# Optimization experiments

Measured on AMD Instinct MI355X. Metric: run time of the kernel, lower is better.

Reference implementation:

```python
import jax, jax.numpy as jnp
import numpy as np

H = 128  # per-direction hidden size; bidirectional output = 256


def sru_layer(x, W, b):
    """One bidirectional SRU layer (use_selu=1).
    x: (L, B, n_in); W: (n_in, 2H*k); b: (4H,) = [f-bias(2H), r-bias(2H)].
    """
    L, B, n_in = x.shape
    k = W.shape[1] // (2 * H)  # 4 if n_in != 2H else 3
    U = (x @ W).reshape(L, B, 2, H, k)  # (L,B,dir,H,k)
    bf = b[: 2 * H].reshape(2, H)
    br = b[2 * H :].reshape(2, H)
    # highway input: learned projection (k==4) or the input itself split per direction
    xp = U[..., 3] if k == 4 else x.reshape(L, B, 2, H)
    # time-reverse the backward direction so a single scan serves both
    Us = jnp.stack([U[:, :, 0, :, :3], U[::-1, :, 1, :, :3]], axis=2)  # (L,B,2,H,3)
    xps = jnp.stack([xp[:, :, 0], xp[::-1, :, 1]], axis=2)  # (L,B,2,H)

    def step(c, t):
        u, xpt = t
        xt = u[..., 0]
        f = jax.nn.sigmoid(u[..., 1] + bf)
        r = jax.nn.sigmoid(u[..., 2] + br)
        c = f * c + (1.0 - f) * xt
        h = r * jax.nn.selu(c) + (1.0 - r) * xpt
        return c, h

    c0 = jnp.zeros((B, 2, H), x.dtype)
    _, hs = jax.lax.scan(step, c0, (Us, xps))  # hs: (L,B,2,H)
    # un-reverse backward direction, concat directions -> (L,B,2H)
    return jnp.concatenate([hs[:, :, 0], hs[::-1, :, 1]], axis=-1)


def setup_inputs() -> dict:
    key = jax.random.key(0)
    ks = jax.random.split(key, 6)
    L, B, D = 1024, 64, 128
    inp = {
        "input": jax.random.normal(ks[0], (L, B, D), jnp.float32),
        "W0": jax.random.normal(ks[1], (D, 4 * 2 * H), jnp.float32) / np.sqrt(D),
        "b0": jnp.zeros((4 * H,), jnp.float32),
        "gamma": jnp.ones((2 * H,), jnp.float32),
        "beta": jnp.zeros((2 * H,), jnp.float32),
    }
    for i, kk in zip((1, 2, 3), ks[2:5]):
        inp[f"W{i}"] = jax.random.normal(kk, (2 * H, 3 * 2 * H), jnp.float32) / np.sqrt(2 * H)
        inp[f"b{i}"] = jnp.zeros((4 * H,), jnp.float32)
    return inp


def reference(input, W0, b0, W1, b1, W2, b2, W3, b3, gamma, beta):
    x = sru_layer(input, W0, b0)
    x = sru_layer(x, W1, b1)
    x = sru_layer(x, W2, b2)
    x = sru_layer(x, W3, b3)  # (L,B,256)
    # permute(1,2,0) + avg_pool1d over full length + squeeze == mean over time
    feats = jnp.mean(x, axis=0)  # (B,256)
    mu = jnp.mean(feats, axis=-1, keepdims=True)
    var = jnp.mean(jnp.square(feats - mu), axis=-1, keepdims=True)
    return (feats - mu) / jnp.sqrt(var + 1e-5) * gamma + beta
```

## Files before the change

kernel.cpp:

```cpp
#include <hip/hip_runtime.h>
#include <math.h>

#define HID 128
#define LSEQ 1024
#define NB 64
#define SUB 32
#define NQG (LSEQ / SUB)
#define NCH 16384

typedef __attribute__((ext_vector_type(4))) float f32x4;
typedef __attribute__((ext_vector_type(8))) short bf16x8;
typedef __attribute__((ext_vector_type(8))) unsigned short u16x8;
typedef __attribute__((ext_vector_type(4))) unsigned short u16x4;

__device__ __forceinline__ unsigned short f2bf(float x) {
    union { float f; unsigned int u; } a; a.f = x;
    unsigned int r = a.u + 0x7FFFu + ((a.u >> 16) & 1u);
    return (unsigned short)(r >> 16);
}
__device__ __forceinline__ float bf2f(unsigned short h) {
    union { float f; unsigned int u; } a; a.u = ((unsigned int)h) << 16;
    return a.f;
}
__device__ __forceinline__ float sigmoidf_(float x) { return 1.0f / (1.0f + __expf(-x)); }
__device__ __forceinline__ float seluf_(float x) {
    const float sc = 1.0507009873554805f, al = 1.6732632423543772f;
    return x > 0.0f ? sc * x : sc * al * (__expf(x) - 1.0f);
}

__device__ __forceinline__ void gload16(const unsigned short* g, unsigned short* l) {
    __builtin_amdgcn_global_load_lds(
        (const __attribute__((address_space(1))) unsigned int*)g,
        (__attribute__((address_space(3))) unsigned int*)l, 16, 0, 0);
}

__global__ __launch_bounds__(256) void conv_wt(const float* __restrict__ W,
                                               unsigned short* __restrict__ Wt,
                                               int K, int N, int kw) {
    int idx = blockIdx.x * 256 + threadIdx.x;
    if (idx >= K * N) return;
    int k = idx / N, n = idx - k * N;
    const int dir = n / (128 * kw);
    const int rem = n - dir * 128 * kw;
    const int h = rem / kw, j = rem - h * kw;
    const int np = dir * 128 * kw + j * 128 + h;
    Wt[(size_t)np * K + k] = f2bf(W[idx]);
}

__global__ __launch_bounds__(256) void conv_in(const float* __restrict__ in,
                                               unsigned short* __restrict__ outp,
                                               int n4) {
    int idx = blockIdx.x * 256 + threadIdx.x;
    if (idx >= n4) return;
    const float4 v = *reinterpret_cast<const float4*>(in + (size_t)idx * 4);
    u16x4 w;
    w[0] = f2bf(v.x); w[1] = f2bf(v.y); w[2] = f2bf(v.z); w[3] = f2bf(v.w);
    *(u16x4*)(outp + (size_t)idx * 4) = w;
}

template <int K, int NC>
__global__ __launch_bounds__(256, 2) void gemm_v9(const unsigned short* __restrict__ A,
                                                  const unsigned short* __restrict__ Bt,
                                                  unsigned short* __restrict__ C) {
    constexpr int NN = NC / 128;
    constexpr int NT = K / 64;
    constexpr int NSTEP = 4 * NT;
    __shared__ __align__(16) unsigned short smB[NT * 8192];

    const int bid = blockIdx.x;
    const int mi = bid & 7;
    const int tt = bid >> 3;
    const int n = tt % NN;
    const int mg = (tt / NN) * 8 + mi;
    const int mb = mg * 512;
    const int n0 = n * 128;

    const int tid = threadIdx.x;
    const int w = tid >> 6, l = tid & 63;
    const int rlo = l & 15, g = l >> 4;
    const int kswz = (rlo & 7) * 8;

#pragma unroll
    for (int kt = 0; kt < NT; ++kt)
#pragma unroll
        for (int cc = 0; cc < 4; ++cc) {
            const int col = cc * 32 + (tid >> 3);
            const int kxb = (tid & 7) ^ ((tid >> 3) & 7);
            gload16(Bt + (size_t)(n0 + col) * K + kt * 64 + kxb * 8,
                    &smB[kt * 8192 + cc * 2048 + tid * 8]);
        }

    const unsigned short* gA = A + ((size_t)mb + w * 32 + rlo) * K + g * 8;

    bf16x8 af[2][2][2];
    auto loadA = [&](int s, int buf) {
        const int mt = s / NT, kt = s % NT;
        const unsigned short* p = gA + (size_t)mt * 128 * K + kt * 64;
#pragma unroll
        for (int mf = 0; mf < 2; ++mf)
#pragma unroll
            for (int kk = 0; kk < 2; ++kk)
                af[buf][mf][kk] = *(const bf16x8*)(p + (size_t)mf * 16 * K + kk * 32);
    };

    loadA(0, 0);
    __syncthreads();

    f32x4 acc[2][8];
#pragma unroll
    for (int s = 0; s < NSTEP; ++s) {
        const int mt = s / NT, kt = s % NT, cur = s & 1;
        if (kt == 0) {
#pragma unroll
            for (int mf = 0; mf < 2; ++mf)
#pragma unroll
                for (int nf = 0; nf < 8; ++nf) acc[mf][nf] = (f32x4){0.f, 0.f, 0.f, 0.f};
        }
        if (s + 1 < NSTEP) loadA(s + 1, cur ^ 1);
#pragma unroll
        for (int kk = 0; kk < 2; ++kk) {
            const int koff = (kk * 32 + g * 8) ^ kswz;
            bf16x8 bff[8];
#pragma unroll
            for (int nf = 0; nf < 8; ++nf)
                bff[nf] = *(const bf16x8*)(&smB[kt * 8192 + (nf * 16 + rlo) * 64 + koff]);
#pragma unroll
            for (int mf = 0; mf < 2; ++mf)
#pragma unroll
                for (int nf = 0; nf < 8; ++nf)
                    acc[mf][nf] = __builtin_amdgcn_mfma_f32_16x16x32_bf16(
                        bff[nf], af[cur][mf][kk], acc[mf][nf], 0, 0, 0);
        }
        if (kt == NT - 1) {
            const int rowb = mb + mt * 128 + w * 32;
#pragma unroll
            for (int mf = 0; mf < 2; ++mf) {
                const size_t rbase = (size_t)(rowb + mf * 16 + rlo) * NC + n0 + g * 4;
#pragma unroll
                for (int nf = 0; nf < 8; ++nf) {
                    u16x4 v;
                    v[0] = f2bf(acc[mf][nf][0]); v[1] = f2bf(acc[mf][nf][1]);
                    v[2] = f2bf(acc[mf][nf][2]); v[3] = f2bf(acc[mf][nf][3]);
                    *(u16x4*)(&C[rbase + nf * 16]) = v;
                }
            }
        }
    }
}

template <int NC>
__global__ __launch_bounds__(256) void scanA(const unsigned short* __restrict__ U,
                                             const float* __restrict__ bias,
                                             float* __restrict__ aArr,
                                             float* __restrict__ bArr,
                                             int dirbase, int dbstride,
                                             int chmask, int chshift, int T) {
    const int gid = blockIdx.x * 256 + threadIdx.x;
    const int fc = gid & chmask;
    const int q = gid >> chshift;
    const int dir = dirbase + (fc >> 13);
    const int b = (fc >> 7) & 63, h = fc & 127;
    const int dbase = (fc >> 13) * dbstride;
    const float bfb = bias[dir * HID + h];

    float aa = 1.0f, cc = 0.0f;
#pragma unroll 4
    for (int i = 0; i < SUB; ++i) {
        const int s = q * SUB + i;
        const int t = dir ? (T - 1 - s) : s;
        const size_t m = (size_t)t * NB + b;
        const float u0 = bf2f(U[m * NC + dbase + h]);
        const float u1 = bf2f(U[m * NC + dbase + 128 + h]);
        const float f = sigmoidf_(u1 + bfb);
        cc = f * cc + (1.0f - f) * u0;
        aa *= f;
    }
    const int fcg = dir * 8192 + (fc & 8191);
    aArr[(size_t)q * NCH + fcg] = aa;
    bArr[(size_t)q * NCH + fcg] = cc;
}

template <int Q>
__global__ __launch_bounds__(256) void scanB(const float* __restrict__ aArr,
                                             const float* __restrict__ bArr,
                                             float* __restrict__ cin,
                                             float* __restrict__ carry,
                                             int init, int fcg0) {
    const int fcg = fcg0 + blockIdx.x * 256 + threadIdx.x;
    float a[Q], bb[Q];
#pragma unroll
    for (int q = 0; q < Q; ++q) {
        a[q]  = aArr[(size_t)q * NCH + fcg];
        bb[q] = bArr[(size_t)q * NCH + fcg];
    }
    float c = init ? 0.0f : carry[fcg];
#pragma unroll
    for (int q = 0; q < Q; ++q) {
        cin[(size_t)q * NCH + fcg] = c;
        c = a[q] * c + bb[q];
    }
    carry[fcg] = c;
}

template <int NC, bool XP_FROM_U, bool ACC>
__global__ __launch_bounds__(256) void scanC(const unsigned short* __restrict__ U,
                                             const unsigned short* __restrict__ Xprev,
                                             const float* __restrict__ bias,
                                             const float* __restrict__ cin,
                                             unsigned short* __restrict__ Xout,
                                             float* __restrict__ part,
                                             int dirbase, int dbstride,
                                             int chmask, int chshift,
                                             int T, int t0, int qg0) {
    const int gid = blockIdx.x * 256 + threadIdx.x;
    const int fc = gid & chmask;
    const int q = gid >> chshift;
    const int dir = dirbase + (fc >> 13);
    const int b = (fc >> 7) & 63, h = fc & 127;
    const int dbase = (fc >> 13) * dbstride;
    const float bfb = bias[dir * HID + h];
    const float brb = bias[2 * HID + dir * HID + h];
    const int fcg = dir * 8192 + (fc & 8191);

    float c = cin[(size_t)q * NCH + fcg];
    float psum = 0.0f;
#pragma unroll 4
    for (int i = 0; i < SUB; ++i) {
        const int s = q * SUB + i;
        const int t = dir ? (T - 1 - s) : s;
        const size_t m = (size_t)t * NB + b;
        const size_t xrow = ((size_t)(t0 + t) * NB + b) * (2 * HID) + dir * HID + h;
        const float u0 = bf2f(U[m * NC + dbase + h]);
        const float u1 = bf2f(U[m * NC + dbase + 128 + h]);
        const float u2 = bf2f(U[m * NC + dbase + 256 + h]);
        float xp;
        if constexpr (XP_FROM_U) xp = bf2f(U[m * NC + dbase + 384 + h]);
        else                     xp = bf2f(Xprev[xrow]);
        const float f = sigmoidf_(u1 + bfb);
        const float r = sigmoidf_(u2 + brb);
        c = f * c + (1.0f - f) * u0;
        const float ho = r * seluf_(c) + (1.0f - r) * xp;
        if constexpr (ACC) psum += ho;
        else               Xout[xrow] = f2bf(ho);
    }
    if constexpr (ACC)
        part[(size_t)(qg0 + q) * (NB * 256) + b * 256 + dir * HID + h] = psum;
}

__global__ __launch_bounds__(256) void pool2(const float* __restrict__ part,
                                             const float* __restrict__ gamma,
                                             const float* __restrict__ beta,
                                             float* __restrict__ out) {
    const int b = blockIdx.x, chn = threadIdx.x;
    float s = 0.0f;
#pragma unroll
    for (int i = 0; i < NQG; ++i) s += part[(size_t)i * (NB * 256) + b * 256 + chn];
    const float feat = s * (1.0f / LSEQ);
    __shared__ float red[256];
    red[chn] = feat; __syncthreads();
    for (int off = 128; off > 0; off >>= 1) { if (chn < off) red[chn] += red[chn + off]; __syncthreads(); }
    const float mu = red[0] * (1.0f / 256.0f);
    __syncthreads();
    const float d = feat - mu;
    red[chn] = d * d; __syncthreads();
    for (int off = 128; off > 0; off >>= 1) { if (chn < off) red[chn] += red[chn + off]; __syncthreads(); }
    const float var = red[0] * (1.0f / 256.0f);
    out[b * 256 + chn] = d * rsqrtf(var + 1e-5f) * gamma[chn] + beta[chn];
}

extern "C" void kernel_launch(void* const* d_in, const int* in_sizes, int n_in,
                              void* d_out, int out_size, void* d_ws, size_t ws_size,
                              hipStream_t stream) {
    const float* input = (const float*)d_in[0];
    const float* gamma = (const float*)d_in[3];
    const float* beta  = (const float*)d_in[4];
    const float* Wl[4] = { (const float*)d_in[1], (const float*)d_in[5],
                           (const float*)d_in[7], (const float*)d_in[9] };
    const float* bl[4] = { (const float*)d_in[2], (const float*)d_in[6],
                           (const float*)d_in[8], (const float*)d_in[10] };
    float* out = (float*)d_out;

    char* base = (char*)d_ws;
    size_t off = 0;
    auto alloc = [&](size_t bytes) { size_t o = off; off = (off + bytes + 255) & ~(size_t)255; return o; };

    unsigned short* Wt[4];
    Wt[0] = (unsigned short*)(base + alloc((size_t)1024 * 128 * 2));
    for (int i = 1; i < 4; ++i) Wt[i] = (unsigned short*)(base + alloc((size_t)768 * 256 * 2));
    unsigned short* Xa = (unsigned short*)(base + alloc((size_t)LSEQ * NB * 256 * 2));
    unsigned short* Xb = (unsigned short*)(base + alloc((size_t)LSEQ * NB * 256 * 2));
    unsigned short* Xc = (unsigned short*)(base + alloc((size_t)LSEQ * NB * 128 * 2));
    float* carry = (float*)(base + alloc((size_t)NCH * 4));
    float* aArr  = (float*)(base + alloc((size_t)32 * NCH * 4));
    float* bArr  = (float*)(base + alloc((size_t)32 * NCH * 4));
    float* cinArr= (float*)(base + alloc((size_t)32 * NCH * 4));
    float* part  = (float*)(base + alloc((size_t)NQG * NB * 256 * 4));
    if (ws_size < off + (1u << 21)) return;
    const size_t uavail = ws_size - off;
    unsigned short* U = (unsigned short*)(base + off);

    conv_in<<<(LSEQ * NB * 128 / 4 + 255) / 256, 256, 0, stream>>>(input, Xc, LSEQ * NB * 128 / 4);
    conv_wt<<<(128 * 1024 + 255) / 256, 256, 0, stream>>>(Wl[0], Wt[0], 128, 1024, 4);
    for (int i = 1; i < 4; ++i)
        conv_wt<<<(256 * 768 + 255) / 256, 256, 0, stream>>>(Wl[i], Wt[i], 256, 768, 3);

    const unsigned short* Xin[4] = { Xc, Xa, Xb, Xa };
    unsigned short* Xout[4] = { Xa, Xb, Xa, nullptr };

    if (uavail >= (size_t)LSEQ * NB * 1024 * 2) {
        const int T = LSEQ, Q = T / SUB;
        const dim3 sgrid(NCH * Q / 256);
        for (int layer = 0; layer < 4; ++layer) {
            const int kw = (layer == 0) ? 4 : 3;
            const int dbstride = 128 * kw;
            if (layer == 0)
                gemm_v9<128, 1024><<<dim3(8 * 128), 256, 0, stream>>>(Xin[0], Wt[0], U);
            else
                gemm_v9<256, 768><<<dim3(6 * 128), 256, 0, stream>>>(Xin[layer], Wt[layer], U);
            if (layer == 0)
                scanA<1024><<<sgrid, 256, 0, stream>>>(U, bl[0], aArr, bArr, 0, dbstride,
                                                       NCH - 1, 14, T);
            else
                scanA<768><<<sgrid, 256, 0, stream>>>(U, bl[layer], aArr, bArr, 0, dbstride,
                                                      NCH - 1, 14, T);
            scanB<32><<<NCH / 256, 256, 0, stream>>>(aArr, bArr, cinArr, carry, 1, 0);
            if (layer == 0)
                scanC<1024, true, false><<<sgrid, 256, 0, stream>>>(
                    U, nullptr, bl[0], cinArr, Xout[0], nullptr, 0, dbstride, NCH - 1, 14, T, 0, 0);
            else if (layer < 3)
                scanC<768, false, false><<<sgrid, 256, 0, stream>>>(
                    U, Xin[layer], bl[layer], cinArr, Xout[layer], nullptr, 0, dbstride,
                    NCH - 1, 14, T, 0, 0);
            else
                scanC<768, false, true><<<sgrid, 256, 0, stream>>>(
                    U, Xin[3], bl[3], cinArr, nullptr, part, 0, dbstride, NCH - 1, 14, T, 0, 0);
        }
    } else {
        int T = 0;
        for (int t = 512; t >= 64; t >>= 1)
            if ((size_t)t * NB * 512 * 2 <= uavail) { T = t; break; }
        if (T == 0) return;
        const int C = LSEQ / T, Q = T / SUB;
        const int nmg = T * NB / 512;
        const dim3 sgrid(8192 * Q / 256);
        for (int layer = 0; layer < 4; ++layer) {
            const int kw = (layer == 0) ? 4 : 3;
            const int K = (layer == 0) ? 128 : 256;
            const int Nc = 128 * kw;
            for (int dir = 0; dir < 2; ++dir) {
                const unsigned short* Bts = Wt[layer] + (size_t)dir * Nc * K;
                for (int cc = 0; cc < C; ++cc) {
                    const int ci = dir ? (C - 1 - cc) : cc;
                    const unsigned short* Ap = Xin[layer] + (size_t)ci * T * NB * K;
                    if (layer == 0)
                        gemm_v9<128, 512><<<dim3(4 * nmg), 256, 0, stream>>>(Ap, Bts, U);
                    else
                        gemm_v9<256, 384><<<dim3(3 * nmg), 256, 0, stream>>>(Ap, Bts, U);
                    if (layer == 0)
                        scanA<512><<<sgrid, 256, 0, stream>>>(U, bl[0], aArr, bArr, dir, 0,
                                                              8191, 13, T);
                    else
                        scanA<384><<<sgrid, 256, 0, stream>>>(U, bl[layer], aArr, bArr, dir, 0,
                                                              8191, 13, T);
                    if (Q == 16)
                        scanB<16><<<32, 256, 0, stream>>>(aArr, bArr, cinArr, carry,
                                                          cc == 0 ? 1 : 0, dir * 8192);
                    else
                        scanB<32><<<32, 256, 0, stream>>>(aArr, bArr, cinArr, carry,
                                                          cc == 0 ? 1 : 0, dir * 8192);
                    if (layer == 0)
                        scanC<512, true, false><<<sgrid, 256, 0, stream>>>(
                            U, nullptr, bl[0], cinArr, Xout[0], nullptr, dir, 0,
                            8191, 13, T, ci * T, ci * Q);
                    else if (layer < 3)
                        scanC<384, false, false><<<sgrid, 256, 0, stream>>>(
                            U, Xin[layer], bl[layer], cinArr, Xout[layer], nullptr, dir, 0,
                            8191, 13, T, ci * T, ci * Q);
                    else
                        scanC<384, false, true><<<sgrid, 256, 0, stream>>>(
                            U, Xin[3], bl[3], cinArr, nullptr, part, dir, 0,
                            8191, 13, T, ci * T, ci * Q);
                }
            }
        }
    }
    pool2<<<NB, 256, 0, stream>>>(part, gamma, beta, out);
}
```

Baseline: 415.7 us.

## Store GEMM output in MFMA-fragment tiled layout and index it from scans

The GEMM epilogue now writes each wave's accumulator fragments as contiguous 16-byte chunks in a tiled, fragment-native layout instead of scattered 8-byte row-major stores. scanA/scanC compute the matching tiled address for each (t,b,h), so consecutive threads read adjacent bf16 elements within a tile. The chunked fallback path for small workspaces is removed, and the kernel now returns early if the full U buffer does not fit. The aim is wider, better-coalesced stores in the GEMM. The cost is more complex scan indexing and possibly less contiguous reads in the scans.

Measured after the change: 634.5 us. 52.6% more time.

```diff
diff --git a/kernel.cpp b/kernel.cpp
--- a/kernel.cpp
+++ b/kernel.cpp
@@ -58,10 +58,11 @@
     *(u16x4*)(outp + (size_t)idx * 4) = w;
 }
 
+
 template <int K, int NC>
-__global__ __launch_bounds__(256, 2) void gemm_v9(const unsigned short* __restrict__ A,
-                                                  const unsigned short* __restrict__ Bt,
-                                                  unsigned short* __restrict__ C) {
+__global__ __launch_bounds__(256, 2) void gemm_v10(const unsigned short* __restrict__ A,
+                                                   const unsigned short* __restrict__ Bt,
+                                                   unsigned short* __restrict__ C) {
     constexpr int NN = NC / 128;
     constexpr int NT = K / 64;
     constexpr int NSTEP = 4 * NT;
@@ -132,61 +133,66 @@
                         bff[nf], af[cur][mf][kk], acc[mf][nf], 0, 0, 0);
         }
         if (kt == NT - 1) {
-            const int rowb = mb + mt * 128 + w * 32;
-#pragma unroll
-            for (int mf = 0; mf < 2; ++mf) {
-                const size_t rbase = (size_t)(rowb + mf * 16 + rlo) * NC + n0 + g * 4;
-#pragma unroll
-                for (int nf = 0; nf < 8; ++nf) {
-                    u16x4 v;
-                    v[0] = f2bf(acc[mf][nf][0]); v[1] = f2bf(acc[mf][nf][1]);
-                    v[2] = f2bf(acc[mf][nf][2]); v[3] = f2bf(acc[mf][nf][3]);
-                    *(u16x4*)(&C[rbase + nf * 16]) = v;
-                }
+            unsigned short* dst =
+                C + (((size_t)(mg * NN + n) * 4 + mt) * 16384) + w * 4096 + l * 8;
+#pragma unroll
+            for (int c2 = 0; c2 < 8; ++c2) {
+                const int mf = c2 >> 2, nf2 = (c2 & 3) * 2;
+                u16x8 v;
+                v[0] = f2bf(acc[mf][nf2][0]);     v[1] = f2bf(acc[mf][nf2][1]);
+                v[2] = f2bf(acc[mf][nf2][2]);     v[3] = f2bf(acc[mf][nf2][3]);
+                v[4] = f2bf(acc[mf][nf2 + 1][0]); v[5] = f2bf(acc[mf][nf2 + 1][1]);
+                v[6] = f2bf(acc[mf][nf2 + 1][2]); v[7] = f2bf(acc[mf][nf2 + 1][3]);
+                *(u16x8*)(dst + (size_t)c2 * 512) = v;
             }
         }
     }
 }
 
-template <int NC>
+
+template <int KW>
 __global__ __launch_bounds__(256) void scanA(const unsigned short* __restrict__ U,
                                              const float* __restrict__ bias,
                                              float* __restrict__ aArr,
-                                             float* __restrict__ bArr,
-                                             int dirbase, int dbstride,
-                                             int chmask, int chshift, int T) {
+                                             float* __restrict__ bArr, int T) {
+    constexpr int NN = 2 * KW;
     const int gid = blockIdx.x * 256 + threadIdx.x;
-    const int fc = gid & chmask;
-    const int q = gid >> chshift;
-    const int dir = dirbase + (fc >> 13);
+    const int fc = gid & (NCH - 1);
+    const int q = gid >> 14;
+    const int dir = fc >> 13;
     const int b = (fc >> 7) & 63, h = fc & 127;
-    const int dbase = (fc >> 13) * dbstride;
     const float bfb = bias[dir * HID + h];
+
+    const int lane = ((h >> 2) & 3) * 16 + (b & 15);
+    const int nf = h >> 4;
+    const int chunk = ((b >> 4) & 1) * 4 + (nf >> 1);
+    const int elem = (nf & 1) * 4 + (h & 3);
+    const size_t sub = (size_t)((b >> 5) * 4096 + chunk * 512 + lane * 8 + elem);
+    const size_t pl = (size_t)dir * KW * 65536;
 
     float aa = 1.0f, cc = 0.0f;
 #pragma unroll 4
     for (int i = 0; i < SUB; ++i) {
         const int s = q * SUB + i;
         const int t = dir ? (T - 1 - s) : s;
-        const size_t m = (size_t)t * NB + b;
-        const float u0 = bf2f(U[m * NC + dbase + h]);
-        const float u1 = bf2f(U[m * NC + dbase + 128 + h]);
+        const size_t base = ((size_t)(t >> 3) * NN + 0) * 65536 +
+                            (size_t)((t >> 1) & 3) * 16384 + (size_t)(t & 1) * 8192 + sub;
+        const float u0 = bf2f(U[base + pl]);
+        const float u1 = bf2f(U[base + pl + 65536]);
         const float f = sigmoidf_(u1 + bfb);
         cc = f * cc + (1.0f - f) * u0;
         aa *= f;
     }
-    const int fcg = dir * 8192 + (fc & 8191);
-    aArr[(size_t)q * NCH + fcg] = aa;
-    bArr[(size_t)q * NCH + fcg] = cc;
+    aArr[(size_t)q * NCH + fc] = aa;
+    bArr[(size_t)q * NCH + fc] = cc;
 }
 
 template <int Q>
 __global__ __launch_bounds__(256) void scanB(const float* __restrict__ aArr,
                                              const float* __restrict__ bArr,
                                              float* __restrict__ cin,
-                                             float* __restrict__ carry,
-                                             int init, int fcg0) {
-    const int fcg = fcg0 + blockIdx.x * 256 + threadIdx.x;
+                                             float* __restrict__ carry, int init) {
+    const int fcg = blockIdx.x * 256 + threadIdx.x;
     float a[Q], bb[Q];
 #pragma unroll
     for (int q = 0; q < Q; ++q) {
@@ -202,39 +208,43 @@
     carry[fcg] = c;
 }
 
-template <int NC, bool XP_FROM_U, bool ACC>
+template <int KW, bool XP_FROM_U, bool ACC>
 __global__ __launch_bounds__(256) void scanC(const unsigned short* __restrict__ U,
                                              const unsigned short* __restrict__ Xprev,
                                              const float* __restrict__ bias,
                                              const float* __restrict__ cin,
                                              unsigned short* __restrict__ Xout,
-                                             float* __restrict__ part,
-                                             int dirbase, int dbstride,
-                                             int chmask, int chshift,
-                                             int T, int t0, int qg0) {
+                                             float* __restrict__ part, int T) {
+    constexpr int NN = 2 * KW;
     const int gid = blockIdx.x * 256 + threadIdx.x;
-    const int fc = gid & chmask;
-    const int q = gid >> chshift;
-    const int dir = dirbase + (fc >> 13);
+    const int fc = gid & (NCH - 1);
+    const int q = gid >> 14;
+    const int dir = fc >> 13;
     const int b = (fc >> 7) & 63, h = fc & 127;
-    const int dbase = (fc >> 13) * dbstride;
     const float bfb = bias[dir * HID + h];
     const float brb = bias[2 * HID + dir * HID + h];
-    const int fcg = dir * 8192 + (fc & 8191);
-
-    float c = cin[(size_t)q * NCH + fcg];
+
+    const int lane = ((h >> 2) & 3) * 16 + (b & 15);
+    const int nf = h >> 4;
+    const int chunk = ((b >> 4) & 1) * 4 + (nf >> 1);
+    const int elem = (nf & 1) * 4 + (h & 3);
+    const size_t sub = (size_t)((b >> 5) * 4096 + chunk * 512 + lane * 8 + elem);
+    const size_t pl = (size_t)dir * KW * 65536;
+
+    float c = cin[(size_t)q * NCH + fc];
     float psum = 0.0f;
 #pragma unroll 4
     for (int i = 0; i < SUB; ++i) {
         const int s = q * SUB + i;
         const int t = dir ? (T - 1 - s) : s;
-        const size_t m = (size_t)t * NB + b;
-        const size_t xrow = ((size_t)(t0 + t) * NB + b) * (2 * HID) + dir * HID + h;
-        const float u0 = bf2f(U[m * NC + dbase + h]);
-        const float u1 = bf2f(U[m * NC + dbase + 128 + h]);
-        const float u2 = bf2f(U[m * NC + dbase + 256 + h]);
+        const size_t base = (size_t)(t >> 3) * NN * 65536 +
+                            (size_t)((t >> 1) & 3) * 16384 + (size_t)(t & 1) * 8192 + sub;
+        const size_t xrow = ((size_t)t * NB + b) * (2 * HID) + dir * HID + h;
+        const float u0 = bf2f(U[base + pl]);
+        const float u1 = bf2f(U[base + pl + 65536]);
+        const float u2 = bf2f(U[base + pl + 2 * 65536]);
         float xp;
-        if constexpr (XP_FROM_U) xp = bf2f(U[m * NC + dbase + 384 + h]);
+        if constexpr (XP_FROM_U) xp = bf2f(U[base + pl + 3 * 65536]);
         else                     xp = bf2f(Xprev[xrow]);
         const float f = sigmoidf_(u1 + bfb);
         const float r = sigmoidf_(u2 + brb);
@@ -244,7 +254,7 @@
         else               Xout[xrow] = f2bf(ho);
     }
     if constexpr (ACC)
-        part[(size_t)(qg0 + q) * (NB * 256) + b * 256 + dir * HID + h] = psum;
+        part[(size_t)q * (NB * 256) + b * 256 + dir * HID + h] = psum;
 }
 
 __global__ __launch_bounds__(256) void pool2(const float* __restrict__ part,
@@ -295,8 +305,8 @@
     float* bArr  = (float*)(base + alloc((size_t)32 * NCH * 4));
     float* cinArr= (float*)(base + alloc((size_t)32 * NCH * 4));
     float* part  = (float*)(base + alloc((size_t)NQG * NB * 256 * 4));
-    if (ws_size < off + (1u << 21)) return;
-    const size_t uavail = ws_size - off;
+    const size_t uavail = (ws_size > off) ? (ws_size - off) : 0;
+    if (uavail < (size_t)LSEQ * NB * 1024 * 2) return;
     unsigned short* U = (unsigned short*)(base + off);
 
     conv_in<<<(LSEQ * NB * 128 / 4 + 255) / 256, 256, 0, stream>>>(input, Xc, LSEQ * NB * 128 / 4);
@@ -307,82 +317,28 @@
     const unsigned short* Xin[4] = { Xc, Xa, Xb, Xa };
     unsigned short* Xout[4] = { Xa, Xb, Xa, nullptr };
 
-    if (uavail >= (size_t)LSEQ * NB * 1024 * 2) {
-        const int T = LSEQ, Q = T / SUB;
-        const dim3 sgrid(NCH * Q / 256);
-        for (int layer = 0; layer < 4; ++layer) {
-            const int kw = (layer == 0) ? 4 : 3;
-            const int dbstride = 128 * kw;
-            if (layer == 0)
-                gemm_v9<128, 1024><<<dim3(8 * 128), 256, 0, stream>>>(Xin[0], Wt[0], U);
-            else
-                gemm_v9<256, 768><<<dim3(6 * 128), 256, 0, stream>>>(Xin[layer], Wt[layer], U);
-            if (layer == 0)
-                scanA<1024><<<sgrid, 256, 0, stream>>>(U, bl[0], aArr, bArr, 0, dbstride,
-                                                       NCH - 1, 14, T);
-            else
-                scanA<768><<<sgrid, 256, 0, stream>>>(U, bl[layer], aArr, bArr, 0, dbstride,
-                                                      NCH - 1, 14, T);
-            scanB<32><<<NCH / 256, 256, 0, stream>>>(aArr, bArr, cinArr, carry, 1, 0);
-            if (layer == 0)
-                scanC<1024, true, false><<<sgrid, 256, 0, stream>>>(
-                    U, nullptr, bl[0], cinArr, Xout[0], nullptr, 0, dbstride, NCH - 1, 14, T, 0, 0);
-            else if (layer < 3)
-                scanC<768, false, false><<<sgrid, 256, 0, stream>>>(
-                    U, Xin[layer], bl[layer], cinArr, Xout[layer], nullptr, 0, dbstride,
-                    NCH - 1, 14, T, 0, 0);
-            else
-                scanC<768, false, true><<<sgrid, 256, 0, stream>>>(
-                    U, Xin[3], bl[3], cinArr, nullptr, part, 0, dbstride, NCH - 1, 14, T, 0, 0);
-        }
-    } else {
-        int T = 0;
-        for (int t = 512; t >= 64; t >>= 1)
-            if ((size_t)t * NB * 512 * 2 <= uavail) { T = t; break; }
-        if (T == 0) return;
-        const int C = LSEQ / T, Q = T / SUB;
-        const int nmg = T * NB / 512;
-        const dim3 sgrid(8192 * Q / 256);
-        for (int layer = 0; layer < 4; ++layer) {
-            const int kw = (layer == 0) ? 4 : 3;
-            const int K = (layer == 0) ? 128 : 256;
-            const int Nc = 128 * kw;
-            for (int dir = 0; dir < 2; ++dir) {
-                const unsigned short* Bts = Wt[layer] + (size_t)dir * Nc * K;
-                for (int cc = 0; cc < C; ++cc) {
-                    const int ci = dir ? (C - 1 - cc) : cc;
-                    const unsigned short* Ap = Xin[layer] + (size_t)ci * T * NB * K;
-                    if (layer == 0)
-                        gemm_v9<128, 512><<<dim3(4 * nmg), 256, 0, stream>>>(Ap, Bts, U);
-                    else
-                        gemm_v9<256, 384><<<dim3(3 * nmg), 256, 0, stream>>>(Ap, Bts, U);
-                    if (layer == 0)
-                        scanA<512><<<sgrid, 256, 0, stream>>>(U, bl[0], aArr, bArr, dir, 0,
-                                                              8191, 13, T);
-                    else
-                        scanA<384><<<sgrid, 256, 0, stream>>>(U, bl[layer], aArr, bArr, dir, 0,
-                                                              8191, 13, T);
-                    if (Q == 16)
-                        scanB<16><<<32, 256, 0, stream>>>(aArr, bArr, cinArr, carry,
-                                                          cc == 0 ? 1 : 0, dir * 8192);
-                    else
-                        scanB<32><<<32, 256, 0, stream>>>(aArr, bArr, cinArr, carry,
-                                                          cc == 0 ? 1 : 0, dir * 8192);
-                    if (layer == 0)
-                        scanC<512, true, false><<<sgrid, 256, 0, stream>>>(
-                            U, nullptr, bl[0], cinArr, Xout[0], nullptr, dir, 0,
-                            8191, 13, T, ci * T, ci * Q);
-                    else if (layer < 3)
-                        scanC<384, false, false><<<sgrid, 256, 0, stream>>>(
-                            U, Xin[layer], bl[layer], cinArr, Xout[layer], nullptr, dir, 0,
-                            8191, 13, T, ci * T, ci * Q);
-                    else
-                        scanC<384, false, true><<<sgrid, 256, 0, stream>>>(
-                            U, Xin[3], bl[3], cinArr, nullptr, part, dir, 0,
-                            8191, 13, T, ci * T, ci * Q);
-                }
-            }
-        }
+    const int T = LSEQ;
+    const dim3 sgrid(NCH * (T / SUB) / 256);
+
+    for (int layer = 0; layer < 4; ++layer) {
+        if (layer == 0)
+            gemm_v10<128, 1024><<<dim3(8 * 128), 256, 0, stream>>>(Xin[0], Wt[0], U);
+        else
+            gemm_v10<256, 768><<<dim3(6 * 128), 256, 0, stream>>>(Xin[layer], Wt[layer], U);
+        if (layer == 0)
+            scanA<4><<<sgrid, 256, 0, stream>>>(U, bl[0], aArr, bArr, T);
+        else
+            scanA<3><<<sgrid, 256, 0, stream>>>(U, bl[layer], aArr, bArr, T);
+        scanB<32><<<NCH / 256, 256, 0, stream>>>(aArr, bArr, cinArr, carry, 1);
+        if (layer == 0)
+            scanC<4, true, false><<<sgrid, 256, 0, stream>>>(U, nullptr, bl[0], cinArr,
+                                                             Xout[0], nullptr, T);
+        else if (layer < 3)
+            scanC<3, false, false><<<sgrid, 256, 0, stream>>>(U, Xin[layer], bl[layer], cinArr,
+                                                              Xout[layer], nullptr, T);
+        else
+            scanC<3, false, true><<<sgrid, 256, 0, stream>>>(U, Xin[3], bl[3], cinArr,
+                                                             nullptr, part, T);
     }
     pool2<<<NB, 256, 0, stream>>>(part, gamma, beta, out);
 }
```
